# Kernel optimization log

Measured on AMD Instinct MI355X. Metric: run time of the kernel, lower is better.

## Reference

```python
import jax, jax.numpy as jnp
import numpy as np

D = 512
H = 16
DH = D // H
N = 1024
R0 = 10.0
K_ITER = 20
LAM = 1.0


def _ln(x, w=None, b=None, eps=1e-5):
    m = x.mean(-1, keepdims=True)
    v = ((x - m) ** 2).mean(-1, keepdims=True)
    y = (x - m) * jax.lax.rsqrt(v + eps)
    if w is not None:
        y = y * w + b
    return y


def setup_inputs() -> dict:
    key = jax.random.key(0)
    ks = jax.random.split(key, 24)
    s = 1.0 / np.sqrt(D)
    inp = {
        'h': jax.random.normal(ks[0], (N, D), jnp.float32),
        'x_res': jax.random.normal(ks[1], (N, 3), jnp.float32) * 5.0,
        'mu': jax.random.uniform(ks[2], (H, N), jnp.float32, 0.1, 1.0),
        'nu': jax.random.uniform(ks[3], (H, N), jnp.float32, 0.1, 1.0),
        'log_u_prev': jnp.zeros((H, N), jnp.float32),
        'log_v_prev': jnp.zeros((H, N), jnp.float32),
        'w_rel_res': jax.random.normal(ks[4], (H, N, N), jnp.float32) * 0.1,
        'w_dist': jax.random.uniform(ks[5], (H,), jnp.float32),
        'pos_bins': jax.random.randint(ks[6], (N, N), 0, 68),
        'geo_gate': jax.random.uniform(ks[7], (H,), jnp.float32),
        'ln_attn_w': jnp.ones((D,), jnp.float32),
        'ln_attn_b': jnp.zeros((D,), jnp.float32),
        'Wq': jax.random.normal(ks[8], (D, D), jnp.float32) * s,
        'Wk': jax.random.normal(ks[9], (D, D), jnp.float32) * s,
        'Wv': jax.random.normal(ks[10], (D, D), jnp.float32) * s,
        'Wg': jax.random.normal(ks[11], (D, D), jnp.float32) * s,
        'Wo': jax.random.normal(ks[12], (D, D), jnp.float32) * s,
        'gamma': jax.random.normal(ks[13], (H,), jnp.float32) * 0.01,
        'ln_ff_w': jnp.ones((D,), jnp.float32),
        'ln_ff_b': jnp.zeros((D,), jnp.float32),
        'W1': jax.random.normal(ks[14], (D, 4 * D), jnp.float32) * s,
        'W3': jax.random.normal(ks[15], (D, 4 * D), jnp.float32) * s,
        'W2': jax.random.normal(ks[16], (4 * D, D), jnp.float32) / np.sqrt(4 * D),
    }
    return inp


def reference(h, x_res, mu, nu, log_u_prev, log_v_prev, w_rel_res, w_dist,
              pos_bins, geo_gate, ln_attn_w, ln_attn_b, Wq, Wk, Wv, Wg, Wo,
              gamma, ln_ff_w, ln_ff_b, W1, W3, W2):
    n = h.shape[0]
    h_n = _ln(h, ln_attn_w, ln_attn_b)
    # projections -> (H, N, d_h)
    Q = (h_n @ Wq).reshape(n, H, DH).transpose(1, 0, 2)
    K = (h_n @ Wk).reshape(n, H, DH).transpose(1, 0, 2)
    V = (h_n @ Wv).reshape(n, H, DH).transpose(1, 0, 2)
    G = (h_n @ Wg).reshape(n, H, DH).transpose(1, 0, 2)
    Q_ln = _ln(Q)
    K_ln = _ln(K)
    content = -jnp.einsum('hid,hjd->hij', Q_ln, K_ln) / np.sqrt(DH)
    pos_bias = w_rel_res  # precomputed (H, N, N)
    d2 = ((x_res[:, None, :] - x_res[None, :, :]) ** 2).sum(-1)
    dist = jnp.sqrt(jnp.maximum(d2, 1e-12))
    f_dist = dist / (R0 + dist)
    eff_w = geo_gate * w_dist
    C = content + pos_bias + eff_w[:, None, None] * f_dist[None]
    # log-domain unbalanced Sinkhorn, per-head eps
    eps_h = jnp.array([0.5] * 4 + [1.0] * 4 + [2.0] * 4 + [4.0] * 4, jnp.float32)
    eps_b = eps_h[:, None, None]
    fac = (LAM / (LAM + eps_h))[:, None]  # (H, 1)
    log_mu = jnp.log(jnp.clip(mu, 1e-8))
    log_nu = jnp.log(jnp.clip(nu, 1e-8))
    M = -C / eps_b  # (H, N, N)

    def step(carry, _):
        lu, lv = carry
        lu = fac * (log_mu - jax.nn.logsumexp(M + lv[:, None, :], axis=2))
        lv = fac * (log_nu - jax.nn.logsumexp(M + lu[:, :, None], axis=1))
        return (lu, lv), None

    (log_u, log_v), _ = jax.lax.scan(jax.checkpoint(step),
                                     (log_u_prev, log_v_prev), None,
                                     length=K_ITER)
    # transport plan and outputs
    T = jnp.exp(M + log_u[:, :, None] + log_v[:, None, :])
    T_norm = T / (T.sum(-1, keepdims=True) + 1e-8)
    o = jax.nn.sigmoid(G) * jnp.einsum('hij,hjd->hid', T_norm, V)
    o = o.transpose(1, 0, 2).reshape(n, D)
    h = h + o @ Wo
    x_centroid = jnp.einsum('hij,jc->hic', T_norm, x_res)  # (H, N, 3)
    delta = x_res[None] - x_centroid
    x_res = x_res + jnp.einsum('h,hnc->nc', gamma, delta)
    # SwiGLU FFN
    ff = _ln(h, ln_ff_w, ln_ff_b)
    h = h + (jax.nn.silu(ff @ W1) * (ff @ W3)) @ W2
    return h, x_res, log_u, log_v
```

## Files before the change

### kernel.cpp

```cpp
#include <hip/hip_runtime.h>
#include <math.h>

#define NTOK 1024
#define DDIM 512

using short8 = __attribute__((ext_vector_type(8))) short;
using f32x4  = __attribute__((ext_vector_type(4))) float;

__device__ __forceinline__ float4 ld4(const float* p){ return *(const float4*)p; }
__device__ __forceinline__ void st4(float* p, float4 v){ *(float4*)p = v; }
__device__ __forceinline__ unsigned short bf16r(float x) {
  unsigned int u = __float_as_uint(x);
  u += 0x7fffu + ((u >> 16) & 1u);
  return (unsigned short)(u >> 16);
}
__device__ __forceinline__ float bf16f(unsigned short h) {
  return __uint_as_float(((unsigned int)h) << 16);
}
__device__ __forceinline__ f32x4 mfma16(short8 a, short8 b, f32x4 c) {
  return __builtin_amdgcn_mfma_f32_16x16x32_bf16(a, b, c, 0, 0, 0);
}

__global__ __launch_bounds__(256) void ln_rows(const float* __restrict__ x,
    const float* __restrict__ w, const float* __restrict__ b, float* __restrict__ y) {
  int row = blockIdx.x, t = threadIdx.x;
  const float* xr = x + ((size_t)row << 9);
  float v0 = xr[t], v1 = xr[t + 256];
  float s = v0 + v1, q = v0*v0 + v1*v1;
  #pragma unroll
  for (int off = 1; off < 64; off <<= 1) { s += __shfl_xor(s, off); q += __shfl_xor(q, off); }
  __shared__ float ls[4], lq[4], mb[2];
  int wv = t >> 6;
  if ((t & 63) == 0) { ls[wv] = s; lq[wv] = q; }
  __syncthreads();
  if (t == 0) {
    float S = ls[0]+ls[1]+ls[2]+ls[3];
    float Q = lq[0]+lq[1]+lq[2]+lq[3];
    float m = S * (1.f/512.f);
    float var = Q * (1.f/512.f) - m*m;
    mb[0] = m; mb[1] = 1.f / sqrtf(var + 1e-5f);
  }
  __syncthreads();
  float m = mb[0], inv = mb[1];
  float* yr = y + ((size_t)row << 9);
  yr[t]       = (v0 - m) * inv * w[t] + b[t];
  yr[t + 256] = (v1 - m) * inv * w[t + 256] + b[t + 256];
}

struct C4 {
  const float *S0, *S1, *S2, *S3;
  unsigned short *D0, *D1, *D2, *D3;
};
__global__ __launch_bounds__(256) void convT(C4 p, int K, int N) {
  __shared__ unsigned short Th[64][68];
  __shared__ unsigned short Tl[64][68];
  int z = blockIdx.z;
  const float* src = (z==0)?p.S0:(z==1)?p.S1:(z==2)?p.S2:p.S3;
  unsigned short* dst = (z==0)?p.D0:(z==1)?p.D1:(z==2)?p.D2:p.D3;
  int nt = blockIdx.x << 6, kt = blockIdx.y << 6;
  int t = threadIdx.x;
  int r = t >> 4, c4 = (t & 15) << 2;
  #pragma unroll
  for (int pp = 0; pp < 4; ++pp) {
    int kk = r + (pp << 4);
    float4 v = ld4(src + (size_t)(kt + kk) * N + nt + c4);
    float vv[4] = {v.x, v.y, v.z, v.w};
    #pragma unroll
    for (int i = 0; i < 4; ++i) {
      unsigned short h = bf16r(vv[i]);
      Th[c4 + i][kk] = h;
      Tl[c4 + i][kk] = bf16r(vv[i] - bf16f(h));
    }
  }
  __syncthreads();
  size_t loff = (size_t)N * K;
  #pragma unroll
  for (int pp = 0; pp < 4; ++pp) {
    int nn = r + (pp << 4);
    ushort4 oh, ol;
    oh.x = Th[nn][c4]; oh.y = Th[nn][c4+1]; oh.z = Th[nn][c4+2]; oh.w = Th[nn][c4+3];
    ol.x = Tl[nn][c4]; ol.y = Tl[nn][c4+1]; ol.z = Tl[nn][c4+2]; ol.w = Tl[nn][c4+3];
    *(ushort4*)(dst + (size_t)(nt + nn) * K + kt + c4) = oh;
    *(ushort4*)(dst + loff + (size_t)(nt + nn) * K + kt + c4) = ol;
  }
}

struct P4 {
  const unsigned short *W0, *W1, *W2, *W3;
  float *C0, *C1, *C2, *C3;
};
template<int MODE>
__global__ __launch_bounds__(256) void gemm_mfma(const float* __restrict__ A,
    P4 p, int Kd, int Nd, int kwin) {
  __shared__ unsigned short Ash[64][72];
  __shared__ unsigned short Asl[64][72];
  __shared__ unsigned short Bsh[64][72];
  __shared__ unsigned short Bsl[64][72];
  int t = threadIdx.x;
  int z = blockIdx.z;
  const unsigned short* W = (z==0)?p.W0:(z==1)?p.W1:(z==2)?p.W2:p.W3;
  float* C = (z==0)?p.C0:(z==1)?p.C1:(z==2)?p.C2:p.C3;
  const unsigned short* Wl = W + (size_t)Nd * Kd;
  int bm = blockIdx.y << 6, bn = blockIdx.x << 6;
  int wid = t >> 6, lane = t & 63;
  int wm = wid >> 1, wn = wid & 1;
  int lr = lane & 15, lk = lane >> 4;
  int r0 = t >> 3, ks = (t & 7) << 3;
  int kbeg = kwin ? z * kwin : 0;
  int kend = kwin ? kbeg + kwin : Kd;
  f32x4 acc[2][2];
  #pragma unroll
  for (int i = 0; i < 2; ++i)
    #pragma unroll
    for (int j = 0; j < 2; ++j)
      #pragma unroll
      for (int r = 0; r < 4; ++r) acc[i][j][r] = 0.f;
  for (int k0 = kbeg; k0 < kend; k0 += 64) {
    float4 a00 = ld4(A + (size_t)(bm + r0) * Kd + k0 + ks);
    float4 a01 = ld4(A + (size_t)(bm + r0) * Kd + k0 + ks + 4);
    float4 a10 = ld4(A + (size_t)(bm + r0 + 32) * Kd + k0 + ks);
    float4 a11 = ld4(A + (size_t)(bm + r0 + 32) * Kd + k0 + ks + 4);
    uint4 b0h = *(const uint4*)(W  + (size_t)(bn + r0) * Kd + k0 + ks);
    uint4 b1h = *(const uint4*)(W  + (size_t)(bn + r0 + 32) * Kd + k0 + ks);
    uint4 b0l = *(const uint4*)(Wl + (size_t)(bn + r0) * Kd + k0 + ks);
    uint4 b1l = *(const uint4*)(Wl + (size_t)(bn + r0 + 32) * Kd + k0 + ks);
    __syncthreads();
    {
      float va[8] = {a00.x,a00.y,a00.z,a00.w,a01.x,a01.y,a01.z,a01.w};
      short8 h8, l8;
      #pragma unroll
      for (int i = 0; i < 8; ++i) {
        unsigned short h = bf16r(va[i]);
        h8[i] = (short)h; l8[i] = (short)bf16r(va[i] - bf16f(h));
      }
      *(short8*)&Ash[r0][ks] = h8;
      *(short8*)&Asl[r0][ks] = l8;
    }
    {
      float va[8] = {a10.x,a10.y,a10.z,a10.w,a11.x,a11.y,a11.z,a11.w};
      short8 h8, l8;
      #pragma unroll
      for (int i = 0; i < 8; ++i) {
        unsigned short h = bf16r(va[i]);
        h8[i] = (short)h; l8[i] = (short)bf16r(va[i] - bf16f(h));
      }
      *(short8*)&Ash[r0 + 32][ks] = h8;
      *(short8*)&Asl[r0 + 32][ks] = l8;
    }
    *(uint4*)&Bsh[r0][ks] = b0h;
    *(uint4*)&Bsh[r0 + 32][ks] = b1h;
    *(uint4*)&Bsl[r0][ks] = b0l;
    *(uint4*)&Bsl[r0 + 32][ks] = b1l;
    __syncthreads();
    #pragma unroll
    for (int s = 0; s < 2; ++s) {
      short8 ah0 = *(const short8*)&Ash[wm*32 + lr][s*32 + lk*8];
      short8 ah1 = *(const short8*)&Ash[wm*32 + 16 + lr][s*32 + lk*8];
      short8 al0 = *(const short8*)&Asl[wm*32 + lr][s*32 + lk*8];
      short8 al1 = *(const short8*)&Asl[wm*32 + 16 + lr][s*32 + lk*8];
      short8 bh0 = *(const short8*)&Bsh[wn*32 + lr][s*32 + lk*8];
      short8 bh1 = *(const short8*)&Bsh[wn*32 + 16 + lr][s*32 + lk*8];
      short8 bl0 = *(const short8*)&Bsl[wn*32 + lr][s*32 + lk*8];
      short8 bl1 = *(const short8*)&Bsl[wn*32 + 16 + lr][s*32 + lk*8];
      acc[0][0] = mfma16(ah0, bh0, acc[0][0]);
      acc[0][1] = mfma16(ah0, bh1, acc[0][1]);
      acc[1][0] = mfma16(ah1, bh0, acc[1][0]);
      acc[1][1] = mfma16(ah1, bh1, acc[1][1]);
      acc[0][0] = mfma16(al0, bh0, acc[0][0]);
      acc[0][1] = mfma16(al0, bh1, acc[0][1]);
      acc[1][0] = mfma16(al1, bh0, acc[1][0]);
      acc[1][1] = mfma16(al1, bh1, acc[1][1]);
      acc[0][0] = mfma16(ah0, bl0, acc[0][0]);
      acc[0][1] = mfma16(ah0, bl1, acc[0][1]);
      acc[1][0] = mfma16(ah1, bl0, acc[1][0]);
      acc[1][1] = mfma16(ah1, bl1, acc[1][1]);
    }
  }
  #pragma unroll
  for (int fm = 0; fm < 2; ++fm)
    #pragma unroll
    for (int fn = 0; fn < 2; ++fn) {
      int n = bn + wn*32 + fn*16 + lr;
      #pragma unroll
      for (int r = 0; r < 4; ++r) {
        int m = bm + wm*32 + fm*16 + lk*4 + r;
        float v = acc[fm][fn][r];
        if (MODE == 0) {
          if (z < 3) C[(((size_t)(n >> 5) << 10) + m) * 32 + (n & 31)] = v;
          else       C[(size_t)m * Nd + n] = v;
        } else {
          C[(size_t)m * Nd + n] = v;
        }
      }
    }
}

__global__ __launch_bounds__(256) void qk_ln_split(const float* __restrict__ Q,
    const float* __restrict__ K, unsigned short* __restrict__ Qh,
    unsigned short* __restrict__ Ql, unsigned short* __restrict__ Kh,
    unsigned short* __restrict__ Kl) {
  const float* P = blockIdx.y ? K : Q;
  unsigned short* Dh = blockIdx.y ? Kh : Qh;
  unsigned short* Dl = blockIdx.y ? Kl : Ql;
  int t = threadIdx.x;
  int row = blockIdx.x * 8 + (t >> 5);
  int l = t & 31;
  const float* p = P + ((size_t)row << 5);
  float x = p[l];
  float s = x, q = x*x;
  #pragma unroll
  for (int off = 16; off; off >>= 1) { s += __shfl_xor(s, off, 32); q += __shfl_xor(q, off, 32); }
  float m = s * (1.f/32.f);
  float var = q * (1.f/32.f) - m*m;
  float inv = 1.f / sqrtf(var + 1e-5f);
  float y = (x - m) * inv;
  unsigned short hi = bf16r(y);
  Dh[((size_t)row << 5) + l] = hi;
  Dl[((size_t)row << 5) + l] = bf16r(y - bf16f(hi));
}

__global__ __launch_bounds__(256) void build_M(const unsigned short* __restrict__ Qh,
    const unsigned short* __restrict__ Ql, const unsigned short* __restrict__ Kh,
    const unsigned short* __restrict__ Kl, const float* __restrict__ wrel,
    const float* __restrict__ xres, const float* __restrict__ wdist,
    const float* __restrict__ ggate, short* __restrict__ Mq) {
  int jt = blockIdx.x, it = blockIdx.y, h = blockIdx.z;
  int t = threadIdx.x;
  __shared__ float xi[64][3], xj[64][3];
  if (t < 64) {
    int gi = (it << 6) + t, gj = (jt << 6) + t;
    xi[t][0] = xres[gi*3]; xi[t][1] = xres[gi*3+1]; xi[t][2] = xres[gi*3+2];
    xj[t][0] = xres[gj*3]; xj[t][1] = xres[gj*3+1]; xj[t][2] = xres[gj*3+2];
  }
  int wid = t >> 6, lane = t & 63;
  int wm = wid >> 1, wn = wid & 1;
  int lr = lane & 15, lk = lane >> 4;
  size_t hb = ((size_t)h << 10);
  short8 ah[2], al[2], bh[2], bl[2];
  #pragma unroll
  for (int fm = 0; fm < 2; ++fm) {
    size_t row = hb + (it << 6) + wm*32 + fm*16 + lr;
    ah[fm] = *(const short8*)(Qh + (row << 5) + lk*8);
    al[fm] = *(const short8*)(Ql + (row << 5) + lk*8);
  }
  #pragma unroll
  for (int fn = 0; fn < 2; ++fn) {
    size_t row = hb + (jt << 6) + wn*32 + fn*16 + lr;
    bh[fn] = *(const short8*)(Kh + (row << 5) + lk*8);
    bl[fn] = *(const short8*)(Kl + (row << 5) + lk*8);
  }
  f32x4 acc[2][2];
  #pragma unroll
  for (int i = 0; i < 2; ++i)
    #pragma unroll
    for (int j = 0; j < 2; ++j)
      #pragma unroll
      for (int r = 0; r < 4; ++r) acc[i][j][r] = 0.f;
  #pragma unroll
  for (int fm = 0; fm < 2; ++fm)
    #pragma unroll
    for (int fn = 0; fn < 2; ++fn) {
      acc[fm][fn] = mfma16(ah[fm], bh[fn], acc[fm][fn]);
      acc[fm][fn] = mfma16(al[fm], bh[fn], acc[fm][fn]);
      acc[fm][fn] = mfma16(ah[fm], bl[fn], acc[fm][fn]);
    }
  __syncthreads();
  float inv_eps = 2.0f / (float)(1 << (h >> 2));
  float effw = ggate[h] * wdist[h];
  const float is32 = 0.17677669529663687f;
  #pragma unroll
  for (int fm = 0; fm < 2; ++fm)
    #pragma unroll
    for (int fn = 0; fn < 2; ++fn) {
      int coll = wn*32 + fn*16 + lr;
      int colg = (jt << 6) + coll;
      float xj0 = xj[coll][0], xj1 = xj[coll][1], xj2 = xj[coll][2];
      #pragma unroll
      for (int i = 0; i < 4; ++i) {
        int rowl = wm*32 + fm*16 + lk*4 + i;
        int rowg = (it << 6) + rowl;
        float dx = xi[rowl][0] - xj0, dy = xi[rowl][1] - xj1, dz = xi[rowl][2] - xj2;
        float d2 = dx*dx + dy*dy + dz*dz;
        float dist = sqrtf(fmaxf(d2, 1e-12f));
        float f = dist / (10.0f + dist);
        size_t base = ((size_t)h << 20) + ((size_t)rowg << 10) + colg;
        float m = (acc[fm][fn][i] * is32 - wrel[base] - effw * f) * inv_eps;
        Mq[base] = (short)__float2int_rn(fminf(fmaxf(m * 256.f, -32000.f), 32000.f));
      }
    }
}

__global__ __launch_bounds__(256) void sink_iter8(const short* __restrict__ Mq,
    const float* __restrict__ lvb, const float* __restrict__ mu,
    float* __restrict__ lu_out, float* __restrict__ part) {
  __shared__ float lds[4][1024];
  __shared__ float logmu[16];
  int bt = blockIdx.x, h = blockIdx.y;
  int t = threadIdx.x, w = t >> 6, lane = t & 63;
  float eps = 0.5f * (float)(1 << (h >> 2));
  float fac = 1.f / (1.f + eps);
  const float qs = 1.f / 256.f;
  int rowbase = bt << 4;
  if (t < 16) logmu[t] = __logf(fmaxf(mu[(h << 10) + rowbase + t], 1e-8f));
  const short* Mh = Mq + ((size_t)h << 20);
  int ib = rowbase + (w << 2);
  short8 qa[4], qb[4];
  #pragma unroll
  for (int k = 0; k < 4; ++k) {
    const short* row = Mh + ((size_t)(ib + k) << 10) + (lane << 3);
    qa[k] = *(const short8*)row;
    qb[k] = *(const short8*)(row + 512);
  }
  float4 lv4[2][2], env[2][2];
  #pragma unroll
  for (int c = 0; c < 2; ++c) {
    const float* lp = lvb + (h << 10) + (c << 9) + (lane << 3);
    lv4[c][0] = ld4(lp);
    lv4[c][1] = ld4(lp + 4);
    #pragma unroll
    for (int hv = 0; hv < 2; ++hv) {
      env[c][hv].x = __expf(-lv4[c][hv].x); env[c][hv].y = __expf(-lv4[c][hv].y);
      env[c][hv].z = __expf(-lv4[c][hv].z); env[c][hv].w = __expf(-lv4[c][hv].w);
    }
  }
  float4 colacc[2][2];
  #pragma unroll
  for (int c = 0; c < 2; ++c)
    #pragma unroll
    for (int hv = 0; hv < 2; ++hv) colacc[c][hv] = make_float4(0.f,0.f,0.f,0.f);
  #pragma unroll
  for (int k = 0; k < 4; ++k) {
    short8 q0 = qa[k], q1 = qb[k];
    float4 e[2][2];
    e[0][0].x = __expf((float)q0[0]*qs + lv4[0][0].x);
    e[0][0].y = __expf((float)q0[1]*qs + lv4[0][0].y);
    e[0][0].z = __expf((float)q0[2]*qs + lv4[0][0].z);
    e[0][0].w = __expf((float)q0[3]*qs + lv4[0][0].w);
    e[0][1].x = __expf((float)q0[4]*qs + lv4[0][1].x);
    e[0][1].y = __expf((float)q0[5]*qs + lv4[0][1].y);
    e[0][1].z = __expf((float)q0[6]*qs + lv4[0][1].z);
    e[0][1].w = __expf((float)q0[7]*qs + lv4[0][1].w);
    e[1][0].x = __expf((float)q1[0]*qs + lv4[1][0].x);
    e[1][0].y = __expf((float)q1[1]*qs + lv4[1][0].y);
    e[1][0].z = __expf((float)q1[2]*qs + lv4[1][0].z);
    e[1][0].w = __expf((float)q1[3]*qs + lv4[1][0].w);
    e[1][1].x = __expf((float)q1[4]*qs + lv4[1][1].x);
    e[1][1].y = __expf((float)q1[5]*qs + lv4[1][1].y);
    e[1][1].z = __expf((float)q1[6]*qs + lv4[1][1].z);
    e[1][1].w = __expf((float)q1[7]*qs + lv4[1][1].w);
    float racc = ((e[0][0].x + e[0][0].y) + (e[0][0].z + e[0][0].w))
               + ((e[0][1].x + e[0][1].y) + (e[0][1].z + e[0][1].w))
               + ((e[1][0].x + e[1][0].y) + (e[1][0].z + e[1][0].w))
               + ((e[1][1].x + e[1][1].y) + (e[1][1].z + e[1][1].w));
    #pragma unroll
    for (int off = 1; off < 64; off <<= 1) racc += __shfl_xor(racc, off);
    float lu = fac * (logmu[(w << 2) + k] - __logf(racc));
    if (lane == 0) lu_out[(h << 10) + ib + k] = lu;
    float s1 = __expf(lu);
    #pragma unroll
    for (int c = 0; c < 2; ++c)
      #pragma unroll
      for (int hv = 0; hv < 2; ++hv) {
        colacc[c][hv].x += s1 * (e[c][hv].x * env[c][hv].x);
        colacc[c][hv].y += s1 * (e[c][hv].y * env[c][hv].y);
        colacc[c][hv].z += s1 * (e[c][hv].z * env[c][hv].z);
        colacc[c][hv].w += s1 * (e[c][hv].w * env[c][hv].w);
      }
  }
  #pragma unroll
  for (int c = 0; c < 2; ++c) {
    st4(&lds[w][(c << 9) + (lane << 3)], colacc[c][0]);
    st4(&lds[w][(c << 9) + (lane << 3) + 4], colacc[c][1]);
  }
  __syncthreads();
  #pragma unroll
  for (int c = 0; c < 4; ++c) {
    int j = t + (c << 8);
    float v = (lds[0][j] + lds[1][j]) + (lds[2][j] + lds[3][j]);
    part[(((size_t)(h << 6) + bt) << 10) + j] = v;
  }
}

__global__ __launch_bounds__(256) void sink_fin(const float* __restrict__ part,
    const float* __restrict__ nu, float* __restrict__ lvb) {
  int cx = blockIdx.x, h = blockIdx.y;
  int t = threadIdx.x;
  float eps = 0.5f * (float)(1 << (h >> 2));
  float fac = 1.f / (1.f + eps);
  int j = (cx << 8) + t;
  float sum = 0.f;
  #pragma unroll 16
  for (int b = 0; b < 64; ++b)
    sum += part[(((size_t)(h << 6) + b) << 10) + j];
  float lv = fac * (__logf(fmaxf(nu[(h << 10) + j], 1e-8f)) - __logf(sum));
  lvb[(h << 10) + j] = lv;
}

__global__ __launch_bounds__(256) void attn_out_v5(const short* __restrict__ Mq,
    const float* __restrict__ lu_g, const float* __restrict__ lv_g,
    const float* __restrict__ V, const float* __restrict__ G,
    const float* __restrict__ xres, float* __restrict__ o_buf, float* __restrict__ xc) {
  __shared__ unsigned short eslab[32][1032];
  __shared__ float lv_s[1024];
  __shared__ float lu_s[32];
  __shared__ float Vs[64][44];
  int rb = blockIdx.x, h = blockIdx.y;
  int t = threadIdx.x;
  int rowbase = rb << 5;
  ((float4*)lv_s)[t] = ld4(lv_g + (h << 10) + (t << 2));
  if (t < 32) lu_s[t] = lu_g[(h << 10) + rowbase + t];
  __syncthreads();
  const short* Mh = Mq + ((size_t)h << 20) + ((size_t)rowbase << 10);
  const float qs = 1.f / 256.f;
  #pragma unroll
  for (int rep = 0; rep < 16; ++rep) {
    int idx = (rep << 8) + t;
    int rr = idx >> 7, c8 = (idx & 127) << 3;
    short8 m8 = *(const short8*)(Mh + ((size_t)rr << 10) + c8);
    float lur = lu_s[rr];
    short8 e8;
    #pragma unroll
    for (int i = 0; i < 8; ++i)
      e8[i] = (short)bf16r(__expf((float)m8[i] * qs + lur + lv_s[c8 + i]));
    *(short8*)&eslab[rr][c8] = e8;
  }
  int r = t >> 3, cg = t & 7;
  float accO[4] = {0.f, 0.f, 0.f, 0.f};
  float rs = 0.f, accX = 0.f;
  for (int jt = 0; jt < 16; ++jt) {
    __syncthreads();
    {
      int vr = t >> 2, dq = (t & 3) << 3;
      const float* vp = V + ((((size_t)h << 10) + (jt << 6) + vr) << 5) + dq;
      st4(&Vs[vr][dq], ld4(vp));
      st4(&Vs[vr][dq + 4], ld4(vp + 4));
    }
    if (t < 64) {
      int j = (jt << 6) + t;
      Vs[t][32] = xres[j*3]; Vs[t][33] = xres[j*3+1]; Vs[t][34] = xres[j*3+2];
    }
    __syncthreads();
    const unsigned short* erow = &eslab[r][jt << 6];
    #pragma unroll
    for (int j8 = 0; j8 < 8; ++j8) {
      short8 e8 = *(const short8*)(erow + (j8 << 3));
      #pragma unroll
      for (int i = 0; i < 8; ++i) {
        int jj = (j8 << 3) + i;
        float e = bf16f((unsigned short)e8[i]);
        float4 v4 = ld4(&Vs[jj][cg << 2]);
        accO[0] += e*v4.x; accO[1] += e*v4.y; accO[2] += e*v4.z; accO[3] += e*v4.w;
        rs += e;
        accX += e * Vs[jj][32 + cg];
      }
    }
  }
  float inv = 1.f / (rs + 1e-8f);
  int i = rowbase + r;
  size_t ga = ((size_t)i << 9) + (h << 5) + (cg << 2);
  float4 g4 = ld4(G + ga);
  float4 o;
  o.x = accO[0]*inv / (1.f + __expf(-g4.x));
  o.y = accO[1]*inv / (1.f + __expf(-g4.y));
  o.z = accO[2]*inv / (1.f + __expf(-g4.z));
  o.w = accO[3]*inv / (1.f + __expf(-g4.w));
  st4(o_buf + ga, o);
  if (cg < 3)
    xc[((size_t)((h << 10) + i)) * 3 + cg] = accX * inv;
}

__global__ void x_update(const float* __restrict__ xres, const float* __restrict__ xc,
    const float* __restrict__ gamma, float* __restrict__ xout) {
  int idx = blockIdx.x * 256 + threadIdx.x;
  if (idx >= 3072) return;
  float x = xres[idx];
  float s = x;
  #pragma unroll
  for (int hh = 0; hh < 16; ++hh) s += gamma[hh] * (x - xc[(size_t)hh * 3072 + idx]);
  xout[idx] = s;
}

__global__ __launch_bounds__(256) void silu_mul(const float* __restrict__ P1,
    const float* __restrict__ P3, float* __restrict__ AB) {
  int i = (blockIdx.x * 256 + threadIdx.x) << 2;
  float4 a = ld4(P1 + i), b = ld4(P3 + i);
  float4 o;
  o.x = a.x / (1.f + __expf(-a.x)) * b.x;
  o.y = a.y / (1.f + __expf(-a.y)) * b.y;
  o.z = a.z / (1.f + __expf(-a.z)) * b.z;
  o.w = a.w / (1.f + __expf(-a.w)) * b.w;
  st4(AB + i, o);
}

__global__ __launch_bounds__(256) void add3(const float* __restrict__ a,
    const float* __restrict__ b, const float* __restrict__ c, float* __restrict__ o) {
  int i = (blockIdx.x * 256 + threadIdx.x) << 2;
  float4 va = ld4(a + i), vb = ld4(b + i), vc = ld4(c + i);
  st4(o + i, make_float4(va.x+vb.x+vc.x, va.y+vb.y+vc.y, va.z+vb.z+vc.z, va.w+vb.w+vc.w));
}

extern "C" void kernel_launch(void* const* d_in, const int* in_sizes, int n_in,
                              void* d_out, int out_size, void* d_ws, size_t ws_size,
                              hipStream_t stream) {
  const float* h_in    = (const float*)d_in[0];
  const float* x_res   = (const float*)d_in[1];
  const float* mu      = (const float*)d_in[2];
  const float* nu      = (const float*)d_in[3];
  const float* lv_prev = (const float*)d_in[5];
  const float* wrel    = (const float*)d_in[6];
  const float* wdist   = (const float*)d_in[7];
  const float* ggate   = (const float*)d_in[9];
  const float* lnaw    = (const float*)d_in[10];
  const float* lnab    = (const float*)d_in[11];
  const float* Wq      = (const float*)d_in[12];
  const float* Wk      = (const float*)d_in[13];
  const float* Wv      = (const float*)d_in[14];
  const float* Wg      = (const float*)d_in[15];
  const float* Wo      = (const float*)d_in[16];
  const float* gamma   = (const float*)d_in[17];
  const float* lnfw    = (const float*)d_in[18];
  const float* lnfb    = (const float*)d_in[19];
  const float* W1      = (const float*)d_in[20];
  const float* W3      = (const float*)d_in[21];
  const float* W2      = (const float*)d_in[22];

  float* out = (float*)d_out;
  float* OUT_H  = out;
  float* OUT_X  = out + 524288;
  float* OUT_LU = out + 527360;
  float* OUT_LV = out + 543744;

  if (ws_size < (size_t)19988480 * sizeof(float)) return;
  float* ws   = (float*)d_ws;
  float* Qb   = ws;
  float* Kb   = ws + 524288;
  float* Vb   = ws + 1048576;
  float* Gb   = ws + 1572864;
  float* Mb   = ws + 2097152;
  float* part = ws + 18874368;
  float* xcb  = ws + 19922944;
  short* Mq   = (short*)Mb;
  float* h_n = Mb;
  unsigned short* WqT = (unsigned short*)(Mb + 524288);
  unsigned short* WkT = (unsigned short*)(Mb + 786432);
  unsigned short* WvT = (unsigned short*)(Mb + 1048576);
  unsigned short* WgT = (unsigned short*)(Mb + 1310720);
  unsigned short* Qhh = (unsigned short*)(Mb + 8388608);
  unsigned short* Qll = (unsigned short*)(Mb + 8650752);
  unsigned short* Khh = (unsigned short*)(Mb + 8912896);
  unsigned short* Kll = (unsigned short*)(Mb + 9175040);
  float* P1 = Mb;
  float* P3 = Mb + 2097152;
  float* ABb = Mb + 4194304;
  unsigned short* W1T = (unsigned short*)(Mb + 6291456);
  unsigned short* W3T = (unsigned short*)(Mb + 7340032);
  unsigned short* W2T = (unsigned short*)(Mb + 8388608);
  unsigned short* WoT = (unsigned short*)(Mb + 9437184);
  float* Pa = Mb + 9699328;
  float* Pb = Mb + 10223616;
  float* o_buf = part;
  float* h2  = Qb;
  float* ffb = Kb;

  ln_rows<<<NTOK, 256, 0, stream>>>(h_in, lnaw, lnab, h_n);
  {
    C4 c = { Wq, Wk, Wv, Wg, WqT, WkT, WvT, WgT };
    convT<<<dim3(8, 8, 4), 256, 0, stream>>>(c, 512, 512);
  }
  {
    P4 p = { WqT, WkT, WvT, WgT, Qb, Kb, Vb, Gb };
    gemm_mfma<0><<<dim3(8, 16, 4), 256, 0, stream>>>(h_n, p, 512, 512, 0);
  }
  qk_ln_split<<<dim3(2048, 2), 256, 0, stream>>>(Qb, Kb, Qhh, Qll, Khh, Kll);
  build_M<<<dim3(16, 16, 16), 256, 0, stream>>>(Qhh, Qll, Khh, Kll, wrel, x_res,
                                                wdist, ggate, Mq);
  hipMemcpyAsync(OUT_LV, lv_prev, 16384 * sizeof(float), hipMemcpyDeviceToDevice, stream);
  for (int it = 0; it < 20; ++it) {
    sink_iter8<<<dim3(64, 16), 256, 0, stream>>>(Mq, OUT_LV, mu, OUT_LU, part);
    sink_fin<<<dim3(4, 16), 256, 0, stream>>>(part, nu, OUT_LV);
  }
  attn_out_v5<<<dim3(32, 16), 256, 0, stream>>>(Mq, OUT_LU, OUT_LV, Vb, Gb, x_res, o_buf, xcb);
  x_update<<<12, 256, 0, stream>>>(x_res, xcb, gamma, OUT_X);

  {
    C4 c = { Wo, nullptr, nullptr, nullptr, WoT, nullptr, nullptr, nullptr };
    convT<<<dim3(8, 8, 1), 256, 0, stream>>>(c, 512, 512);
  }
  {
    C4 c = { W1, W3, nullptr, nullptr, W1T, W3T, nullptr, nullptr };
    convT<<<dim3(32, 8, 2), 256, 0, stream>>>(c, 512, 2048);
  }
  {
    C4 c = { W2, nullptr, nullptr, nullptr, W2T, nullptr, nullptr, nullptr };
    convT<<<dim3(8, 32, 1), 256, 0, stream>>>(c, 2048, 512);
  }
  {
    P4 p = { WoT, WoT, nullptr, nullptr, Pa, Pb, nullptr, nullptr };
    gemm_mfma<1><<<dim3(8, 16, 2), 256, 0, stream>>>(o_buf, p, 512, 512, 256);
  }
  add3<<<512, 256, 0, stream>>>(Pa, Pb, h_in, h2);
  ln_rows<<<NTOK, 256, 0, stream>>>(h2, lnfw, lnfb, ffb);
  {
    P4 p = { W1T, W3T, nullptr, nullptr, P1, P3, nullptr, nullptr };
    gemm_mfma<1><<<dim3(32, 16, 2), 256, 0, stream>>>(ffb, p, 512, 2048, 0);
  }
  silu_mul<<<2048, 256, 0, stream>>>(P1, P3, ABb);
  {
    P4 p = { W2T, W2T, nullptr, nullptr, Pa, Pb, nullptr, nullptr };
    gemm_mfma<1><<<dim3(8, 16, 2), 256, 0, stream>>>(ABb, p, 2048, 512, 1024);
  }
  add3<<<512, 256, 0, stream>>>(Pa, Pb, h2, OUT_H);
}
```

Before: 449.2 us.

## Fuse FFN epilogues, rewrite attention output with MFMA, remap sinkhorn block order

Several independent changes. The residual add is fused into the FFN layernorm. The W1 and W3 GEMMs are fused into one kernel that applies SiLU-multiply in its epilogue, which removes the P1/P3 round trip and the separate silu kernel. The attention-output kernel now computes the exp(M+u+v)·[V|x|1] product with bf16 MFMA instead of scalar FMAs, using a prepacked transposed B matrix, and the row sum comes from a ones column. The sinkhorn row kernel uses a 1D grid with a remapped head order, presumably for cache locality. Workspace offsets are reshuffled, and the Wo convT call now passes W2 as a second source that is not used.

```diff
diff --git a/kernel.cpp b/kernel.cpp
--- a/kernel.cpp
+++ b/kernel.cpp
@@ -45,6 +45,36 @@
   float* yr = y + ((size_t)row << 9);
   yr[t]       = (v0 - m) * inv * w[t] + b[t];
   yr[t + 256] = (v1 - m) * inv * w[t + 256] + b[t + 256];
+}
+
+__global__ __launch_bounds__(256) void ln_rows3(const float* __restrict__ pa,
+    const float* __restrict__ pb, const float* __restrict__ hi,
+    const float* __restrict__ w, const float* __restrict__ b,
+    float* __restrict__ hsum, float* __restrict__ y) {
+  int row = blockIdx.x, t = threadIdx.x;
+  size_t base = ((size_t)row << 9);
+  float v0 = pa[base + t] + pb[base + t] + hi[base + t];
+  float v1 = pa[base + t + 256] + pb[base + t + 256] + hi[base + t + 256];
+  float s = v0 + v1, q = v0*v0 + v1*v1;
+  #pragma unroll
+  for (int off = 1; off < 64; off <<= 1) { s += __shfl_xor(s, off); q += __shfl_xor(q, off); }
+  __shared__ float ls[4], lq[4], mb[2];
+  int wv = t >> 6;
+  if ((t & 63) == 0) { ls[wv] = s; lq[wv] = q; }
+  __syncthreads();
+  if (t == 0) {
+    float S = ls[0]+ls[1]+ls[2]+ls[3];
+    float Q = lq[0]+lq[1]+lq[2]+lq[3];
+    float m = S * (1.f/512.f);
+    float var = Q * (1.f/512.f) - m*m;
+    mb[0] = m; mb[1] = 1.f / sqrtf(var + 1e-5f);
+  }
+  __syncthreads();
+  float m = mb[0], inv = mb[1];
+  hsum[base + t] = v0;
+  hsum[base + t + 256] = v1;
+  y[base + t]       = (v0 - m) * inv * w[t] + b[t];
+  y[base + t + 256] = (v1 - m) * inv * w[t + 256] + b[t + 256];
 }
 
 struct C4 {
@@ -195,6 +225,127 @@
     }
 }
 
+__global__ __launch_bounds__(256) void gemm_w13(const float* __restrict__ A,
+    const unsigned short* __restrict__ W1T, const unsigned short* __restrict__ W3T,
+    float* __restrict__ AB) {
+  __shared__ unsigned short Ash[64][72];
+  __shared__ unsigned short Asl[64][72];
+  __shared__ unsigned short B1h[64][72];
+  __shared__ unsigned short B1l[64][72];
+  __shared__ unsigned short B3h[64][72];
+  __shared__ unsigned short B3l[64][72];
+  const int Kd = 512, Nd = 2048;
+  int t = threadIdx.x;
+  const unsigned short* W1l = W1T + (size_t)Nd * Kd;
+  const unsigned short* W3l = W3T + (size_t)Nd * Kd;
+  int bm = blockIdx.y << 6, bn = blockIdx.x << 6;
+  int wid = t >> 6, lane = t & 63;
+  int wm = wid >> 1, wn = wid & 1;
+  int lr = lane & 15, lk = lane >> 4;
+  int r0 = t >> 3, ks = (t & 7) << 3;
+  f32x4 acc1[2][2], acc3[2][2];
+  #pragma unroll
+  for (int i = 0; i < 2; ++i)
+    #pragma unroll
+    for (int j = 0; j < 2; ++j)
+      #pragma unroll
+      for (int r = 0; r < 4; ++r) { acc1[i][j][r] = 0.f; acc3[i][j][r] = 0.f; }
+  for (int k0 = 0; k0 < Kd; k0 += 64) {
+    float4 a00 = ld4(A + (size_t)(bm + r0) * Kd + k0 + ks);
+    float4 a01 = ld4(A + (size_t)(bm + r0) * Kd + k0 + ks + 4);
+    float4 a10 = ld4(A + (size_t)(bm + r0 + 32) * Kd + k0 + ks);
+    float4 a11 = ld4(A + (size_t)(bm + r0 + 32) * Kd + k0 + ks + 4);
+    uint4 c0h = *(const uint4*)(W1T + (size_t)(bn + r0) * Kd + k0 + ks);
+    uint4 c1h = *(const uint4*)(W1T + (size_t)(bn + r0 + 32) * Kd + k0 + ks);
+    uint4 c0l = *(const uint4*)(W1l + (size_t)(bn + r0) * Kd + k0 + ks);
+    uint4 c1l = *(const uint4*)(W1l + (size_t)(bn + r0 + 32) * Kd + k0 + ks);
+    uint4 d0h = *(const uint4*)(W3T + (size_t)(bn + r0) * Kd + k0 + ks);
+    uint4 d1h = *(const uint4*)(W3T + (size_t)(bn + r0 + 32) * Kd + k0 + ks);
+    uint4 d0l = *(const uint4*)(W3l + (size_t)(bn + r0) * Kd + k0 + ks);
+    uint4 d1l = *(const uint4*)(W3l + (size_t)(bn + r0 + 32) * Kd + k0 + ks);
+    __syncthreads();
+    {
+      float va[8] = {a00.x,a00.y,a00.z,a00.w,a01.x,a01.y,a01.z,a01.w};
+      short8 h8, l8;
+      #pragma unroll
+      for (int i = 0; i < 8; ++i) {
+        unsigned short h = bf16r(va[i]);
+        h8[i] = (short)h; l8[i] = (short)bf16r(va[i] - bf16f(h));
+      }
+      *(short8*)&Ash[r0][ks] = h8;
+      *(short8*)&Asl[r0][ks] = l8;
+    }
+    {
+      float va[8] = {a10.x,a10.y,a10.z,a10.w,a11.x,a11.y,a11.z,a11.w};
+      short8 h8, l8;
+      #pragma unroll
+      for (int i = 0; i < 8; ++i) {
+        unsigned short h = bf16r(va[i]);
+        h8[i] = (short)h; l8[i] = (short)bf16r(va[i] - bf16f(h));
+      }
+      *(short8*)&Ash[r0 + 32][ks] = h8;
+      *(short8*)&Asl[r0 + 32][ks] = l8;
+    }
+    *(uint4*)&B1h[r0][ks] = c0h;  *(uint4*)&B1h[r0 + 32][ks] = c1h;
+    *(uint4*)&B1l[r0][ks] = c0l;  *(uint4*)&B1l[r0 + 32][ks] = c1l;
+    *(uint4*)&B3h[r0][ks] = d0h;  *(uint4*)&B3h[r0 + 32][ks] = d1h;
+    *(uint4*)&B3l[r0][ks] = d0l;  *(uint4*)&B3l[r0 + 32][ks] = d1l;
+    __syncthreads();
+    #pragma unroll
+    for (int s = 0; s < 2; ++s) {
+      short8 ah0 = *(const short8*)&Ash[wm*32 + lr][s*32 + lk*8];
+      short8 ah1 = *(const short8*)&Ash[wm*32 + 16 + lr][s*32 + lk*8];
+      short8 al0 = *(const short8*)&Asl[wm*32 + lr][s*32 + lk*8];
+      short8 al1 = *(const short8*)&Asl[wm*32 + 16 + lr][s*32 + lk*8];
+      short8 p0h = *(const short8*)&B1h[wn*32 + lr][s*32 + lk*8];
+      short8 p1h = *(const short8*)&B1h[wn*32 + 16 + lr][s*32 + lk*8];
+      short8 p0l = *(const short8*)&B1l[wn*32 + lr][s*32 + lk*8];
+      short8 p1l = *(const short8*)&B1l[wn*32 + 16 + lr][s*32 + lk*8];
+      acc1[0][0] = mfma16(ah0, p0h, acc1[0][0]);
+      acc1[0][1] = mfma16(ah0, p1h, acc1[0][1]);
+      acc1[1][0] = mfma16(ah1, p0h, acc1[1][0]);
+      acc1[1][1] = mfma16(ah1, p1h, acc1[1][1]);
+      acc1[0][0] = mfma16(al0, p0h, acc1[0][0]);
+      acc1[0][1] = mfma16(al0, p1h, acc1[0][1]);
+      acc1[1][0] = mfma16(al1, p0h, acc1[1][0]);
+      acc1[1][1] = mfma16(al1, p1h, acc1[1][1]);
+      acc1[0][0] = mfma16(ah0, p0l, acc1[0][0]);
+      acc1[0][1] = mfma16(ah0, p1l, acc1[0][1]);
+      acc1[1][0] = mfma16(ah1, p0l, acc1[1][0]);
+      acc1[1][1] = mfma16(ah1, p1l, acc1[1][1]);
+      short8 q0h = *(const short8*)&B3h[wn*32 + lr][s*32 + lk*8];
+      short8 q1h = *(const short8*)&B3h[wn*32 + 16 + lr][s*32 + lk*8];
+      short8 q0l = *(const short8*)&B3l[wn*32 + lr][s*32 + lk*8];
+      short8 q1l = *(const short8*)&B3l[wn*32 + 16 + lr][s*32 + lk*8];
+      acc3[0][0] = mfma16(ah0, q0h, acc3[0][0]);
+      acc3[0][1] = mfma16(ah0, q1h, acc3[0][1]);
+      acc3[1][0] = mfma16(ah1, q0h, acc3[1][0]);
+      acc3[1][1] = mfma16(ah1, q1h, acc3[1][1]);
+      acc3[0][0] = mfma16(al0, q0h, acc3[0][0]);
+      acc3[0][1] = mfma16(al0, q1h, acc3[0][1]);
+      acc3[1][0] = mfma16(al1, q0h, acc3[1][0]);
+      acc3[1][1] = mfma16(al1, q1h, acc3[1][1]);
+      acc3[0][0] = mfma16(ah0, q0l, acc3[0][0]);
+      acc3[0][1] = mfma16(ah0, q1l, acc3[0][1]);
+      acc3[1][0] = mfma16(ah1, q0l, acc3[1][0]);
+      acc3[1][1] = mfma16(ah1, q1l, acc3[1][1]);
+    }
+  }
+  #pragma unroll
+  for (int fm = 0; fm < 2; ++fm)
+    #pragma unroll
+    for (int fn = 0; fn < 2; ++fn) {
+      int n = bn + wn*32 + fn*16 + lr;
+      #pragma unroll
+      for (int r = 0; r < 4; ++r) {
+        int m = bm + wm*32 + fm*16 + lk*4 + r;
+        float p1 = acc1[fm][fn][r];
+        float p3 = acc3[fm][fn][r];
+        AB[(size_t)m * Nd + n] = p1 / (1.f + __expf(-p1)) * p3;
+      }
+    }
+}
+
 __global__ __launch_bounds__(256) void qk_ln_split(const float* __restrict__ Q,
     const float* __restrict__ K, unsigned short* __restrict__ Qh,
     unsigned short* __restrict__ Ql, unsigned short* __restrict__ Kh,
@@ -295,7 +446,9 @@
     float* __restrict__ lu_out, float* __restrict__ part) {
   __shared__ float lds[4][1024];
   __shared__ float logmu[16];
-  int bt = blockIdx.x, h = blockIdx.y;
+  int id = blockIdx.x;
+  int h = (((id >> 3) & 1) << 3) | (id & 7);
+  int bt = id >> 4;
   int t = threadIdx.x, w = t >> 6, lane = t & 63;
   float eps = 0.5f * (float)(1 << (h >> 2));
   float fac = 1.f / (1.f + eps);
@@ -396,77 +549,123 @@
   lvb[(h << 10) + j] = lv;
 }
 
-__global__ __launch_bounds__(256) void attn_out_v5(const short* __restrict__ Mq,
-    const float* __restrict__ lu_g, const float* __restrict__ lv_g,
-    const float* __restrict__ V, const float* __restrict__ G,
-    const float* __restrict__ xres, float* __restrict__ o_buf, float* __restrict__ xc) {
-  __shared__ unsigned short eslab[32][1032];
+__global__ __launch_bounds__(256) void attn_prep(const float* __restrict__ V,
+    const float* __restrict__ xres, unsigned short* __restrict__ Bt) {
+  int jb = blockIdx.x, h = blockIdx.y;
+  int t = threadIdx.x;
+  #pragma unroll
+  for (int rep = 0; rep < 12; ++rep) {
+    int idx = t + (rep << 8);
+    int jl = idx & 63, c = idx >> 6;
+    int j = (jb << 6) + jl;
+    float val;
+    if (c < 32)      val = V[((((size_t)h << 10) + j) << 5) + c];
+    else if (c < 35) val = xres[j * 3 + (c - 32)];
+    else if (c == 35) val = 1.f;
+    else              val = 0.f;
+    Bt[(((size_t)h * 48 + c) << 10) + j] = bf16r(val);
+  }
+}
+
+__global__ __launch_bounds__(256) void attn_out_v6(const short* __restrict__ Mq,
+    const unsigned short* __restrict__ Bt, const float* __restrict__ lu_g,
+    const float* __restrict__ lv_g, const float* __restrict__ G,
+    float* __restrict__ o_buf, float* __restrict__ xc) {
   __shared__ float lv_s[1024];
   __shared__ float lu_s[32];
-  __shared__ float Vs[64][44];
+  __shared__ float red[3][64][24];
+  __shared__ float rs_s[32];
   int rb = blockIdx.x, h = blockIdx.y;
-  int t = threadIdx.x;
+  int t = threadIdx.x, w = t >> 6, lane = t & 63;
+  int lr = lane & 15, lk = lane >> 4;
   int rowbase = rb << 5;
   ((float4*)lv_s)[t] = ld4(lv_g + (h << 10) + (t << 2));
   if (t < 32) lu_s[t] = lu_g[(h << 10) + rowbase + t];
   __syncthreads();
+  const float qs = 1.f / 256.f;
+  float lu0 = lu_s[lr], lu1 = lu_s[16 + lr];
   const short* Mh = Mq + ((size_t)h << 20) + ((size_t)rowbase << 10);
-  const float qs = 1.f / 256.f;
-  #pragma unroll
-  for (int rep = 0; rep < 16; ++rep) {
-    int idx = (rep << 8) + t;
-    int rr = idx >> 7, c8 = (idx & 127) << 3;
-    short8 m8 = *(const short8*)(Mh + ((size_t)rr << 10) + c8);
-    float lur = lu_s[rr];
-    short8 e8;
-    #pragma unroll
-    for (int i = 0; i < 8; ++i)
-      e8[i] = (short)bf16r(__expf((float)m8[i] * qs + lur + lv_s[c8 + i]));
-    *(short8*)&eslab[rr][c8] = e8;
-  }
-  int r = t >> 3, cg = t & 7;
-  float accO[4] = {0.f, 0.f, 0.f, 0.f};
-  float rs = 0.f, accX = 0.f;
-  for (int jt = 0; jt < 16; ++jt) {
-    __syncthreads();
-    {
-      int vr = t >> 2, dq = (t & 3) << 3;
-      const float* vp = V + ((((size_t)h << 10) + (jt << 6) + vr) << 5) + dq;
-      st4(&Vs[vr][dq], ld4(vp));
-      st4(&Vs[vr][dq + 4], ld4(vp + 4));
-    }
-    if (t < 64) {
-      int j = (jt << 6) + t;
-      Vs[t][32] = xres[j*3]; Vs[t][33] = xres[j*3+1]; Vs[t][34] = xres[j*3+2];
-    }
-    __syncthreads();
-    const unsigned short* erow = &eslab[r][jt << 6];
-    #pragma unroll
-    for (int j8 = 0; j8 < 8; ++j8) {
-      short8 e8 = *(const short8*)(erow + (j8 << 3));
-      #pragma unroll
-      for (int i = 0; i < 8; ++i) {
-        int jj = (j8 << 3) + i;
-        float e = bf16f((unsigned short)e8[i]);
-        float4 v4 = ld4(&Vs[jj][cg << 2]);
-        accO[0] += e*v4.x; accO[1] += e*v4.y; accO[2] += e*v4.z; accO[3] += e*v4.w;
-        rs += e;
-        accX += e * Vs[jj][32 + cg];
-      }
-    }
-  }
-  float inv = 1.f / (rs + 1e-8f);
-  int i = rowbase + r;
-  size_t ga = ((size_t)i << 9) + (h << 5) + (cg << 2);
-  float4 g4 = ld4(G + ga);
-  float4 o;
-  o.x = accO[0]*inv / (1.f + __expf(-g4.x));
-  o.y = accO[1]*inv / (1.f + __expf(-g4.y));
-  o.z = accO[2]*inv / (1.f + __expf(-g4.z));
-  o.w = accO[3]*inv / (1.f + __expf(-g4.w));
-  st4(o_buf + ga, o);
-  if (cg < 3)
-    xc[((size_t)((h << 10) + i)) * 3 + cg] = accX * inv;
+  const unsigned short* Bh = Bt + (((size_t)h * 48) << 10);
+  f32x4 acc[2][3];
+  #pragma unroll
+  for (int i = 0; i < 2; ++i)
+    #pragma unroll
+    for (int j = 0; j < 3; ++j)
+      #pragma unroll
+      for (int r = 0; r < 4; ++r) acc[i][j][r] = 0.f;
+  for (int step = 0; step < 8; ++step) {
+    int ks = (step << 2) | w;
+    int j0 = (ks << 5) + (lk << 3);
+    short8 m0 = *(const short8*)(Mh + ((size_t)lr << 10) + j0);
+    short8 m1 = *(const short8*)(Mh + ((size_t)(16 + lr) << 10) + j0);
+    short8 a0, a1;
+    #pragma unroll
+    for (int i = 0; i < 8; ++i) {
+      float lvv = lv_s[j0 + i];
+      a0[i] = (short)bf16r(__expf((float)m0[i] * qs + lu0 + lvv));
+      a1[i] = (short)bf16r(__expf((float)m1[i] * qs + lu1 + lvv));
+    }
+    short8 b0 = *(const short8*)(Bh + ((size_t)lr << 10) + j0);
+    short8 b1 = *(const short8*)(Bh + ((size_t)(16 + lr) << 10) + j0);
+    short8 b2 = *(const short8*)(Bh + ((size_t)(32 + lr) << 10) + j0);
+    acc[0][0] = mfma16(a0, b0, acc[0][0]);
+    acc[0][1] = mfma16(a0, b1, acc[0][1]);
+    acc[0][2] = mfma16(a0, b2, acc[0][2]);
+    acc[1][0] = mfma16(a1, b0, acc[1][0]);
+    acc[1][1] = mfma16(a1, b1, acc[1][1]);
+    acc[1][2] = mfma16(a1, b2, acc[1][2]);
+  }
+  if (w) {
+    #pragma unroll
+    for (int fm = 0; fm < 2; ++fm)
+      #pragma unroll
+      for (int fn = 0; fn < 3; ++fn)
+        #pragma unroll
+        for (int i = 0; i < 4; ++i)
+          red[w - 1][lane][(fm * 3 + fn) * 4 + i] = acc[fm][fn][i];
+  }
+  __syncthreads();
+  if (w == 0) {
+    #pragma unroll
+    for (int fm = 0; fm < 2; ++fm)
+      #pragma unroll
+      for (int fn = 0; fn < 3; ++fn)
+        #pragma unroll
+        for (int i = 0; i < 4; ++i)
+          acc[fm][fn][i] += red[0][lane][(fm*3+fn)*4+i] + red[1][lane][(fm*3+fn)*4+i]
+                          + red[2][lane][(fm*3+fn)*4+i];
+    if (lr == 3) {
+      #pragma unroll
+      for (int fm = 0; fm < 2; ++fm)
+        #pragma unroll
+        for (int i = 0; i < 4; ++i)
+          rs_s[fm*16 + lk*4 + i] = acc[fm][2][i];
+    }
+    #pragma unroll
+    for (int fm = 0; fm < 2; ++fm)
+      #pragma unroll
+      for (int fn = 0; fn < 2; ++fn)
+        #pragma unroll
+        for (int i = 0; i < 4; ++i) {
+          int rl = fm*16 + lk*4 + i;
+          int row = rowbase + rl;
+          int col = fn*16 + lr;
+          float inv = 1.f / (rs_s[rl] + 1e-8f);
+          size_t ga = ((size_t)row << 9) + h*32 + col;
+          float g = G[ga];
+          o_buf[ga] = acc[fm][fn][i] * inv / (1.f + __expf(-g));
+        }
+    if (lr < 3) {
+      #pragma unroll
+      for (int fm = 0; fm < 2; ++fm)
+        #pragma unroll
+        for (int i = 0; i < 4; ++i) {
+          int rl = fm*16 + lk*4 + i;
+          int row = rowbase + rl;
+          xc[((size_t)((h << 10) + row)) * 3 + lr] = acc[fm][2][i] / (rs_s[rl] + 1e-8f);
+        }
+    }
+  }
 }
 
 __global__ void x_update(const float* __restrict__ xres, const float* __restrict__ xc,
@@ -478,18 +677,6 @@
   #pragma unroll
   for (int hh = 0; hh < 16; ++hh) s += gamma[hh] * (x - xc[(size_t)hh * 3072 + idx]);
   xout[idx] = s;
-}
-
-__global__ __launch_bounds__(256) void silu_mul(const float* __restrict__ P1,
-    const float* __restrict__ P3, float* __restrict__ AB) {
-  int i = (blockIdx.x * 256 + threadIdx.x) << 2;
-  float4 a = ld4(P1 + i), b = ld4(P3 + i);
-  float4 o;
-  o.x = a.x / (1.f + __expf(-a.x)) * b.x;
-  o.y = a.y / (1.f + __expf(-a.y)) * b.y;
-  o.z = a.z / (1.f + __expf(-a.z)) * b.z;
-  o.w = a.w / (1.f + __expf(-a.w)) * b.w;
-  st4(AB + i, o);
 }
 
 __global__ __launch_bounds__(256) void add3(const float* __restrict__ a,
@@ -549,15 +736,15 @@
   unsigned short* Qll = (unsigned short*)(Mb + 8650752);
   unsigned short* Khh = (unsigned short*)(Mb + 8912896);
   unsigned short* Kll = (unsigned short*)(Mb + 9175040);
-  float* P1 = Mb;
-  float* P3 = Mb + 2097152;
+  unsigned short* Bt = (unsigned short*)(Mb + 8388608);
+  float* P1unused = Mb; (void)P1unused;
   float* ABb = Mb + 4194304;
-  unsigned short* W1T = (unsigned short*)(Mb + 6291456);
-  unsigned short* W3T = (unsigned short*)(Mb + 7340032);
-  unsigned short* W2T = (unsigned short*)(Mb + 8388608);
-  unsigned short* WoT = (unsigned short*)(Mb + 9437184);
-  float* Pa = Mb + 9699328;
-  float* Pb = Mb + 10223616;
+  unsigned short* W1T = (unsigned short*)(Mb + 0);
+  unsigned short* W3T = (unsigned short*)(Mb + 1048576);
+  unsigned short* W2T = (unsigned short*)(Mb + 2097152);
+  unsigned short* WoT = (unsigned short*)(Mb + 3145728);
+  float* Pa = Mb + 6291456;
+  float* Pb = Mb + 6815744;
   float* o_buf = part;
   float* h2  = Qb;
   float* ffb = Kb;
@@ -574,16 +761,17 @@
   qk_ln_split<<<dim3(2048, 2), 256, 0, stream>>>(Qb, Kb, Qhh, Qll, Khh, Kll);
   build_M<<<dim3(16, 16, 16), 256, 0, stream>>>(Qhh, Qll, Khh, Kll, wrel, x_res,
                                                 wdist, ggate, Mq);
+  attn_prep<<<dim3(16, 16), 256, 0, stream>>>(Vb, x_res, Bt);
   hipMemcpyAsync(OUT_LV, lv_prev, 16384 * sizeof(float), hipMemcpyDeviceToDevice, stream);
   for (int it = 0; it < 20; ++it) {
-    sink_iter8<<<dim3(64, 16), 256, 0, stream>>>(Mq, OUT_LV, mu, OUT_LU, part);
+    sink_iter8<<<1024, 256, 0, stream>>>(Mq, OUT_LV, mu, OUT_LU, part);
     sink_fin<<<dim3(4, 16), 256, 0, stream>>>(part, nu, OUT_LV);
   }
-  attn_out_v5<<<dim3(32, 16), 256, 0, stream>>>(Mq, OUT_LU, OUT_LV, Vb, Gb, x_res, o_buf, xcb);
+  attn_out_v6<<<dim3(32, 16), 256, 0, stream>>>(Mq, Bt, OUT_LU, OUT_LV, Gb, o_buf, xcb);
   x_update<<<12, 256, 0, stream>>>(x_res, xcb, gamma, OUT_X);
 
   {
-    C4 c = { Wo, nullptr, nullptr, nullptr, WoT, nullptr, nullptr, nullptr };
+    C4 c = { Wo, W2, nullptr, nullptr, WoT, nullptr, nullptr, nullptr };
     convT<<<dim3(8, 8, 1), 256, 0, stream>>>(c, 512, 512);
   }
   {
@@ -598,13 +786,8 @@
     P4 p = { WoT, WoT, nullptr, nullptr, Pa, Pb, nullptr, nullptr };
     gemm_mfma<1><<<dim3(8, 16, 2), 256, 0, stream>>>(o_buf, p, 512, 512, 256);
   }
-  add3<<<512, 256, 0, stream>>>(Pa, Pb, h_in, h2);
-  ln_rows<<<NTOK, 256, 0, stream>>>(h2, lnfw, lnfb, ffb);
-  {
-    P4 p = { W1T, W3T, nullptr, nullptr, P1, P3, nullptr, nullptr };
-    gemm_mfma<1><<<dim3(32, 16, 2), 256, 0, stream>>>(ffb, p, 512, 2048, 0);
-  }
-  silu_mul<<<2048, 256, 0, stream>>>(P1, P3, ABb);
+  ln_rows3<<<NTOK, 256, 0, stream>>>(Pa, Pb, h_in, lnfw, lnfb, h2, ffb);
+  gemm_w13<<<dim3(32, 16), 256, 0, stream>>>(ffb, W1T, W3T, ABb);
   {
     P4 p = { W2T, W2T, nullptr, nullptr, Pa, Pb, nullptr, nullptr };
     gemm_mfma<1><<<dim3(8, 16, 2), 256, 0, stream>>>(ABb, p, 2048, 512, 1024);
```

Result: faster. 406.8 us (-9.4%).
